# Performance work log

Measured on AMD Instinct MI355X. Metric: run time of the kernel, lower is better.

## Reference

```python
import jax, jax.numpy as jnp
import numpy as np

B, D, H, R = 64, 256, 512, 32
CLIP_VAL = 50.0


def setup_inputs() -> dict:
    key = jax.random.key(0)
    ks = jax.random.split(key, 12)
    inp = {
        "x": jax.random.normal(ks[0], (B, D), jnp.float32),
        "h": jax.random.normal(ks[1], (B, H), jnp.float32) * 0.1,
        "v": jax.random.normal(ks[2], (B, H), jnp.float32) * 0.1,
        "dU": jax.random.normal(ks[3], (B, H, H), jnp.float32) * 0.01,
        "trace_e": jax.random.normal(ks[4], (B, H), jnp.float32) * 0.1,
        "trace_E": jax.random.normal(ks[5], (B, H, H), jnp.float32) * 0.01,
        # parameters (per reset_parameter: xavier inits, zero biases)
        "x2h_w": jax.random.normal(ks[6], (H + R, D), jnp.float32) * (2.0 / (D + H + R)) ** 0.5,
        "x2h_b": jnp.zeros((H + R,), jnp.float32),
        "h2h_w": jax.random.normal(ks[7], (H + R, H), jnp.float32) * 1.5 * (2.0 / (H + H + R)) ** 0.5,
        "h2h_b": jnp.zeros((H + R,), jnp.float32),
        "alpha": jnp.ones((1, H, H), jnp.float32),
        "tau_v": -2.0 * jnp.ones((1, H), jnp.float32),
        "tau_e": -2.5 * jnp.ones((1, H), jnp.float32),
        "tau_U": -3.5 * jnp.ones((1,), jnp.float32),
        "tau_E": -3.5 * jnp.ones((1,), jnp.float32),
    }
    return inp


def _sgru_step(x, h, v, dU, trace_e, trace_E,
               x2h_w, x2h_b, h2h_w, h2h_b, alpha, tau_v, tau_e, tau_U, tau_E):
    Wx = x @ x2h_w.T + x2h_b            # [B, H+R]
    Wh = h @ h2h_w.T + h2h_b            # [B, H+R]
    alpha_r = jax.nn.relu(alpha)        # [1, H, H]
    # plastic fast-weight contribution: (relu(alpha)*dU) @ h
    plastic = jnp.einsum('bij,bj->bi', alpha_r * dU, h)  # [B, H]
    dv = Wx[:, :H] + Wh[:, :H] + plastic
    sv = jax.nn.sigmoid(tau_v)          # [1, H]
    v_new = (1.0 - sv) * v + sv * dv
    new_h = jax.nn.relu(v_new)          # activation='relu'
    # neuromodulatory scalar per batch element (sum over mod_rank channels)
    mod = jax.nn.relu(Wx[:, H:] + Wh[:, H:]).sum(axis=-1)  # [B]
    se = jax.nn.sigmoid(tau_e)
    new_trace_e = (1.0 - se) * trace_e + se * h             # [B, H]
    sE = jax.nn.sigmoid(tau_E)
    # antisymmetric eligibility trace update via outer products
    outer = new_h[:, :, None] * trace_e[:, None, :] - new_trace_e[:, :, None] * h[:, None, :]
    new_trace_E = (1.0 - sE) * trace_E + sE * outer         # [B, H, H]
    sU = jax.nn.sigmoid(tau_U)
    dU_new = (1.0 - sU) * dU + sU * mod[:, None, None] * new_trace_E
    # clip fast weights so total recurrent weight stays within [-clip, clip]
    W_hh = h2h_w[:H, :]                                     # [H, H]
    denom = alpha_r + 1e-8
    upper = jax.nn.relu(CLIP_VAL - W_hh) / denom            # [1, H, H]
    lower = -jax.nn.relu(CLIP_VAL + W_hh) / denom
    dU_new = jnp.maximum(jnp.minimum(dU_new, upper), lower)
    return v_new, new_h, dU_new, new_trace_e, new_trace_E


def reference(x, h, v, dU, trace_e, trace_E,
              x2h_w, x2h_b, h2h_w, h2h_b, alpha, tau_v, tau_e, tau_U, tau_E):
    return _sgru_step(x, h, v, dU, trace_e, trace_E,
                      x2h_w, x2h_b, h2h_w, h2h_b, alpha, tau_v, tau_e, tau_U, tau_E)
```

## Files before the change

### kernel.cpp

```cpp
#include <hip/hip_runtime.h>

#define BB 64
#define DD 256
#define HH 512
#define RR 32
#define CLIPV 50.0f

#define OUT_V   0
#define OUT_H   (BB * HH)
#define OUT_DU  (2 * BB * HH)
#define OUT_TE  (2 * BB * HH + BB * HH * HH)
#define OUT_TEE (3 * BB * HH + BB * HH * HH)

__device__ __forceinline__ float sigmoidf_(float x) {
    return 1.0f / (1.0f + expf(-x));
}

__global__ __launch_bounds__(256) void k_small(
    const float* __restrict__ x, const float* __restrict__ h, const float* __restrict__ v,
    const float* __restrict__ dU, const float* __restrict__ trace_e,
    const float* __restrict__ x2h_w, const float* __restrict__ x2h_b,
    const float* __restrict__ h2h_w, const float* __restrict__ h2h_b,
    const float* __restrict__ alpha,
    const float* __restrict__ tau_v, const float* __restrict__ tau_e,
    float* __restrict__ out, float* __restrict__ mod_ws)
{
    const int wave = blockIdx.x * 4 + (threadIdx.x >> 6);
    const int lane = threadIdx.x & 63;
    const int b = wave / (HH + RR);
    const int i = wave - b * (HH + RR);

    float4 xv = *reinterpret_cast<const float4*>(x + b * DD + lane * 4);
    float4 wv = *reinterpret_cast<const float4*>(x2h_w + i * DD + lane * 4);
    float s  = xv.x * wv.x + xv.y * wv.y + xv.z * wv.z + xv.w * wv.w;
    float pl = 0.0f;

    if (i < HH) {
        const float* dUrow = dU + (b * HH + i) * HH;
        const float* arow  = alpha + i * HH;
        #pragma unroll
        for (int p = 0; p < 2; ++p) {
            const int j0 = p * 256 + lane * 4;
            float4 hv  = *reinterpret_cast<const float4*>(h + b * HH + j0);
            float4 whv = *reinterpret_cast<const float4*>(h2h_w + i * HH + j0);
            s += hv.x * whv.x + hv.y * whv.y + hv.z * whv.z + hv.w * whv.w;
            float4 duv = *reinterpret_cast<const float4*>(dUrow + j0);
            float4 av  = *reinterpret_cast<const float4*>(arow + j0);
            pl += fmaxf(av.x, 0.f) * duv.x * hv.x
                + fmaxf(av.y, 0.f) * duv.y * hv.y
                + fmaxf(av.z, 0.f) * duv.z * hv.z
                + fmaxf(av.w, 0.f) * duv.w * hv.w;
        }
    } else {
        #pragma unroll
        for (int p = 0; p < 2; ++p) {
            const int j0 = p * 256 + lane * 4;
            float4 hv  = *reinterpret_cast<const float4*>(h + b * HH + j0);
            float4 whv = *reinterpret_cast<const float4*>(h2h_w + i * HH + j0);
            s += hv.x * whv.x + hv.y * whv.y + hv.z * whv.z + hv.w * whv.w;
        }
    }

    #pragma unroll
    for (int off = 32; off > 0; off >>= 1) {
        s  += __shfl_xor(s, off, 64);
        pl += __shfl_xor(pl, off, 64);
    }

    if (lane == 0) {
        s += x2h_b[i] + h2h_b[i];
        if (i < HH) {
            const int bi = b * HH + i;
            const float dv = s + pl;
            const float sv = sigmoidf_(tau_v[i]);
            const float vn = (1.f - sv) * v[bi] + sv * dv;
            out[OUT_V + bi] = vn;
            out[OUT_H + bi] = fmaxf(vn, 0.f);
            const float se = sigmoidf_(tau_e[i]);
            out[OUT_TE + bi] = (1.f - se) * trace_e[bi] + se * h[bi];
        } else {
            atomicAdd(mod_ws + b, fmaxf(s, 0.f));
        }
    }
}

__global__ __launch_bounds__(256) void k_big(
    const float* __restrict__ dU, const float* __restrict__ trace_E,
    const float* __restrict__ h, const float* __restrict__ trace_e,
    const float* __restrict__ alpha, const float* __restrict__ h2h_w,
    const float* __restrict__ tau_U, const float* __restrict__ tau_E,
    const float* __restrict__ mod_ws, float* __restrict__ out)
{
    const float sU = sigmoidf_(tau_U[0]);
    const float sE = sigmoidf_(tau_E[0]);
    const float omU = 1.f - sU, omE = 1.f - sE;
    const float* __restrict__ new_h  = out + OUT_H;
    const float* __restrict__ new_te = out + OUT_TE;
    float* __restrict__ out_dU = out + OUT_DU;
    float* __restrict__ out_tE = out + OUT_TEE;

    const int total = (BB * HH * HH) / 4;
    for (int idx = blockIdx.x * blockDim.x + threadIdx.x; idx < total;
         idx += gridDim.x * blockDim.x) {
        const int flat = idx << 2;
        const int b   = flat >> 18;
        const int rem = flat & ((1 << 18) - 1);
        const int i   = rem >> 9;
        const int j   = rem & (HH - 1);

        float4 tE = *reinterpret_cast<const float4*>(trace_E + flat);
        float4 du = *reinterpret_cast<const float4*>(dU + flat);
        float4 al = *reinterpret_cast<const float4*>(alpha + rem);
        float4 W  = *reinterpret_cast<const float4*>(h2h_w + rem);
        float4 hv = *reinterpret_cast<const float4*>(h + b * HH + j);
        float4 te = *reinterpret_cast<const float4*>(trace_e + b * HH + j);
        const float nh   = new_h[b * HH + i];
        const float nte  = new_te[b * HH + i];
        const float smod = sU * mod_ws[b];

        float4 rE, rU;
        #define COMP(c)                                                  \
        {                                                                \
            const float outer = nh * te.c - nte * hv.c;                  \
            const float nE    = omE * tE.c + sE * outer;                 \
            float dnew        = omU * du.c + smod * nE;                  \
            const float ar    = fmaxf(al.c, 0.f);                        \
            const float inv   = 1.0f / (ar + 1e-8f);                     \
            const float up    = fmaxf(CLIPV - W.c, 0.f) * inv;           \
            const float lo    = -fmaxf(CLIPV + W.c, 0.f) * inv;          \
            rE.c = nE;                                                   \
            rU.c = fmaxf(fminf(dnew, up), lo);                           \
        }
        COMP(x) COMP(y) COMP(z) COMP(w)
        #undef COMP

        *reinterpret_cast<float4*>(out_tE + flat) = rE;
        *reinterpret_cast<float4*>(out_dU + flat) = rU;
    }
}

extern "C" void kernel_launch(void* const* d_in, const int* in_sizes, int n_in,
                              void* d_out, int out_size, void* d_ws, size_t ws_size,
                              hipStream_t stream) {
    const float* x       = (const float*)d_in[0];
    const float* h       = (const float*)d_in[1];
    const float* v       = (const float*)d_in[2];
    const float* dU      = (const float*)d_in[3];
    const float* trace_e = (const float*)d_in[4];
    const float* trace_E = (const float*)d_in[5];
    const float* x2h_w   = (const float*)d_in[6];
    const float* x2h_b   = (const float*)d_in[7];
    const float* h2h_w   = (const float*)d_in[8];
    const float* h2h_b   = (const float*)d_in[9];
    const float* alpha   = (const float*)d_in[10];
    const float* tau_v   = (const float*)d_in[11];
    const float* tau_e   = (const float*)d_in[12];
    const float* tau_U   = (const float*)d_in[13];
    const float* tau_E   = (const float*)d_in[14];
    float* out    = (float*)d_out;
    float* mod_ws = (float*)d_ws;

    hipMemsetAsync(d_ws, 0, BB * sizeof(float), stream);

    const int waves = BB * (HH + RR);
    k_small<<<waves / 4, 256, 0, stream>>>(x, h, v, dU, trace_e, x2h_w, x2h_b,
                                           h2h_w, h2h_b, alpha, tau_v, tau_e,
                                           out, mod_ws);
    k_big<<<2048, 256, 0, stream>>>(dU, trace_E, h, trace_e, alpha, h2h_w,
                                    tau_U, tau_E, mod_ws, out);
}
```

Measured before the change: 288.0 us.

## Fuse plastic matvec with eligibility/fast-weight update to read dU once

New measurement: 281.6 us. 1.02x faster.

```diff
diff --git a/kernel.cpp b/kernel.cpp
--- a/kernel.cpp
+++ b/kernel.cpp
@@ -16,49 +16,77 @@
     return 1.0f / (1.0f + expf(-x));
 }
 
-__global__ __launch_bounds__(256) void k_small(
+__global__ __launch_bounds__(256) void k_mod(
+    const float* __restrict__ x, const float* __restrict__ h,
+    const float* __restrict__ x2h_w, const float* __restrict__ x2h_b,
+    const float* __restrict__ h2h_w, const float* __restrict__ h2h_b,
+    float* __restrict__ mod_ws)
+{
+    const int wave = blockIdx.x * 4 + (threadIdx.x >> 6);
+    const int lane = threadIdx.x & 63;
+    const int b = wave >> 5;
+    const int r = wave & (RR - 1);
+    const int i = HH + r;
+
+    float4 xv = *reinterpret_cast<const float4*>(x + b * DD + lane * 4);
+    float4 wv = *reinterpret_cast<const float4*>(x2h_w + i * DD + lane * 4);
+    float s = xv.x * wv.x + xv.y * wv.y + xv.z * wv.z + xv.w * wv.w;
+
+    #pragma unroll
+    for (int p = 0; p < 2; ++p) {
+        const int j0 = p * 256 + lane * 4;
+        float4 hv  = *reinterpret_cast<const float4*>(h + b * HH + j0);
+        float4 whv = *reinterpret_cast<const float4*>(h2h_w + i * HH + j0);
+        s += hv.x * whv.x + hv.y * whv.y + hv.z * whv.z + hv.w * whv.w;
+    }
+
+    #pragma unroll
+    for (int off = 32; off > 0; off >>= 1)
+        s += __shfl_xor(s, off, 64);
+
+    if (lane == 0) {
+        s += x2h_b[i] + h2h_b[i];
+        atomicAdd(mod_ws + b, fmaxf(s, 0.f));
+    }
+}
+
+__global__ __launch_bounds__(256) void k_fused(
     const float* __restrict__ x, const float* __restrict__ h, const float* __restrict__ v,
     const float* __restrict__ dU, const float* __restrict__ trace_e,
+    const float* __restrict__ trace_E,
     const float* __restrict__ x2h_w, const float* __restrict__ x2h_b,
     const float* __restrict__ h2h_w, const float* __restrict__ h2h_b,
     const float* __restrict__ alpha,
     const float* __restrict__ tau_v, const float* __restrict__ tau_e,
-    float* __restrict__ out, float* __restrict__ mod_ws)
+    const float* __restrict__ tau_U, const float* __restrict__ tau_E,
+    const float* __restrict__ mod_ws, float* __restrict__ out)
 {
     const int wave = blockIdx.x * 4 + (threadIdx.x >> 6);
     const int lane = threadIdx.x & 63;
-    const int b = wave / (HH + RR);
-    const int i = wave - b * (HH + RR);
+    const int b = wave >> 9;
+    const int i = wave & (HH - 1);
+    const int bi = b * HH + i;
 
     float4 xv = *reinterpret_cast<const float4*>(x + b * DD + lane * 4);
     float4 wv = *reinterpret_cast<const float4*>(x2h_w + i * DD + lane * 4);
     float s  = xv.x * wv.x + xv.y * wv.y + xv.z * wv.z + xv.w * wv.w;
     float pl = 0.0f;
 
-    if (i < HH) {
-        const float* dUrow = dU + (b * HH + i) * HH;
-        const float* arow  = alpha + i * HH;
-        #pragma unroll
-        for (int p = 0; p < 2; ++p) {
-            const int j0 = p * 256 + lane * 4;
-            float4 hv  = *reinterpret_cast<const float4*>(h + b * HH + j0);
-            float4 whv = *reinterpret_cast<const float4*>(h2h_w + i * HH + j0);
-            s += hv.x * whv.x + hv.y * whv.y + hv.z * whv.z + hv.w * whv.w;
-            float4 duv = *reinterpret_cast<const float4*>(dUrow + j0);
-            float4 av  = *reinterpret_cast<const float4*>(arow + j0);
-            pl += fmaxf(av.x, 0.f) * duv.x * hv.x
-                + fmaxf(av.y, 0.f) * duv.y * hv.y
-                + fmaxf(av.z, 0.f) * duv.z * hv.z
-                + fmaxf(av.w, 0.f) * duv.w * hv.w;
-        }
-    } else {
-        #pragma unroll
-        for (int p = 0; p < 2; ++p) {
-            const int j0 = p * 256 + lane * 4;
-            float4 hv  = *reinterpret_cast<const float4*>(h + b * HH + j0);
-            float4 whv = *reinterpret_cast<const float4*>(h2h_w + i * HH + j0);
-            s += hv.x * whv.x + hv.y * whv.y + hv.z * whv.z + hv.w * whv.w;
-        }
+    float4 hv[2], wh[2], du[2], av[2], te[2];
+    #pragma unroll
+    for (int p = 0; p < 2; ++p) {
+        const int j0 = p * 256 + lane * 4;
+        hv[p] = *reinterpret_cast<const float4*>(h + b * HH + j0);
+        wh[p] = *reinterpret_cast<const float4*>(h2h_w + i * HH + j0);
+        du[p] = *reinterpret_cast<const float4*>(dU + (size_t)bi * HH + j0);
+        av[p] = *reinterpret_cast<const float4*>(alpha + i * HH + j0);
+        te[p] = *reinterpret_cast<const float4*>(trace_e + b * HH + j0);
+        s += hv[p].x * wh[p].x + hv[p].y * wh[p].y
+           + hv[p].z * wh[p].z + hv[p].w * wh[p].w;
+        pl += fmaxf(av[p].x, 0.f) * du[p].x * hv[p].x
+            + fmaxf(av[p].y, 0.f) * du[p].y * hv[p].y
+            + fmaxf(av[p].z, 0.f) * du[p].z * hv[p].z
+            + fmaxf(av[p].w, 0.f) * du[p].w * hv[p].w;
     }
 
     #pragma unroll
@@ -67,75 +95,58 @@
         pl += __shfl_xor(pl, off, 64);
     }
 
+    s += x2h_b[i] + h2h_b[i];
+    const float dv = s + pl;
+    const float sv = sigmoidf_(tau_v[i]);
+    const float vn = (1.f - sv) * v[bi] + sv * dv;
+    const float nh = fmaxf(vn, 0.f);
+    const float se = sigmoidf_(tau_e[i]);
+    const float nte = (1.f - se) * trace_e[bi] + se * h[bi];
+
     if (lane == 0) {
-        s += x2h_b[i] + h2h_b[i];
-        if (i < HH) {
-            const int bi = b * HH + i;
-            const float dv = s + pl;
-            const float sv = sigmoidf_(tau_v[i]);
-            const float vn = (1.f - sv) * v[bi] + sv * dv;
-            out[OUT_V + bi] = vn;
-            out[OUT_H + bi] = fmaxf(vn, 0.f);
-            const float se = sigmoidf_(tau_e[i]);
-            out[OUT_TE + bi] = (1.f - se) * trace_e[bi] + se * h[bi];
-        } else {
-            atomicAdd(mod_ws + b, fmaxf(s, 0.f));
-        }
+        out[OUT_V  + bi] = vn;
+        out[OUT_H  + bi] = nh;
+        out[OUT_TE + bi] = nte;
     }
-}
 
-__global__ __launch_bounds__(256) void k_big(
-    const float* __restrict__ dU, const float* __restrict__ trace_E,
-    const float* __restrict__ h, const float* __restrict__ trace_e,
-    const float* __restrict__ alpha, const float* __restrict__ h2h_w,
-    const float* __restrict__ tau_U, const float* __restrict__ tau_E,
-    const float* __restrict__ mod_ws, float* __restrict__ out)
-{
-    const float sU = sigmoidf_(tau_U[0]);
-    const float sE = sigmoidf_(tau_E[0]);
+    const float sU  = sigmoidf_(tau_U[0]);
+    const float sE  = sigmoidf_(tau_E[0]);
     const float omU = 1.f - sU, omE = 1.f - sE;
-    const float* __restrict__ new_h  = out + OUT_H;
-    const float* __restrict__ new_te = out + OUT_TE;
+    const float smod = sU * mod_ws[b];
+
     float* __restrict__ out_dU = out + OUT_DU;
     float* __restrict__ out_tE = out + OUT_TEE;
 
-    const int total = (BB * HH * HH) / 4;
-    for (int idx = blockIdx.x * blockDim.x + threadIdx.x; idx < total;
-         idx += gridDim.x * blockDim.x) {
-        const int flat = idx << 2;
-        const int b   = flat >> 18;
-        const int rem = flat & ((1 << 18) - 1);
-        const int i   = rem >> 9;
-        const int j   = rem & (HH - 1);
-
+    #pragma unroll
+    for (int p = 0; p < 2; ++p) {
+        const int j0 = p * 256 + lane * 4;
+        const size_t flat = (size_t)bi * HH + j0;
         float4 tE = *reinterpret_cast<const float4*>(trace_E + flat);
-        float4 du = *reinterpret_cast<const float4*>(dU + flat);
-        float4 al = *reinterpret_cast<const float4*>(alpha + rem);
-        float4 W  = *reinterpret_cast<const float4*>(h2h_w + rem);
-        float4 hv = *reinterpret_cast<const float4*>(h + b * HH + j);
-        float4 te = *reinterpret_cast<const float4*>(trace_e + b * HH + j);
-        const float nh   = new_h[b * HH + i];
-        const float nte  = new_te[b * HH + i];
-        const float smod = sU * mod_ws[b];
 
         float4 rE, rU;
         #define COMP(c)                                                  \
         {                                                                \
-            const float outer = nh * te.c - nte * hv.c;                  \
+            const float outer = nh * te[p].c - nte * hv[p].c;            \
             const float nE    = omE * tE.c + sE * outer;                 \
-            float dnew        = omU * du.c + smod * nE;                  \
-            const float ar    = fmaxf(al.c, 0.f);                        \
+            const float dnew  = omU * du[p].c + smod * nE;               \
+            const float ar    = fmaxf(av[p].c, 0.f);                     \
             const float inv   = 1.0f / (ar + 1e-8f);                     \
-            const float up    = fmaxf(CLIPV - W.c, 0.f) * inv;           \
-            const float lo    = -fmaxf(CLIPV + W.c, 0.f) * inv;          \
+            const float up    = fmaxf(CLIPV - wh[p].c, 0.f) * inv;       \
+            const float lo    = -fmaxf(CLIPV + wh[p].c, 0.f) * inv;      \
             rE.c = nE;                                                   \
             rU.c = fmaxf(fminf(dnew, up), lo);                           \
         }
         COMP(x) COMP(y) COMP(z) COMP(w)
         #undef COMP
 
-        *reinterpret_cast<float4*>(out_tE + flat) = rE;
-        *reinterpret_cast<float4*>(out_dU + flat) = rU;
+        __builtin_nontemporal_store(rE.x, out_tE + flat + 0);
+        __builtin_nontemporal_store(rE.y, out_tE + flat + 1);
+        __builtin_nontemporal_store(rE.z, out_tE + flat + 2);
+        __builtin_nontemporal_store(rE.w, out_tE + flat + 3);
+        __builtin_nontemporal_store(rU.x, out_dU + flat + 0);
+        __builtin_nontemporal_store(rU.y, out_dU + flat + 1);
+        __builtin_nontemporal_store(rU.z, out_dU + flat + 2);
+        __builtin_nontemporal_store(rU.w, out_dU + flat + 3);
     }
 }
 
@@ -162,10 +173,9 @@
 
     hipMemsetAsync(d_ws, 0, BB * sizeof(float), stream);
 
-    const int waves = BB * (HH + RR);
-    k_small<<<waves / 4, 256, 0, stream>>>(x, h, v, dU, trace_e, x2h_w, x2h_b,
-                                           h2h_w, h2h_b, alpha, tau_v, tau_e,
-                                           out, mod_ws);
-    k_big<<<2048, 256, 0, stream>>>(dU, trace_E, h, trace_e, alpha, h2h_w,
-                                    tau_U, tau_E, mod_ws, out);
+    k_mod<<<512, 256, 0, stream>>>(x, h, x2h_w, x2h_b, h2h_w, h2h_b, mod_ws);
+
+    k_fused<<<8192, 256, 0, stream>>>(x, h, v, dU, trace_e, trace_E,
+                                      x2h_w, x2h_b, h2h_w, h2h_b, alpha,
+                                      tau_v, tau_e, tau_U, tau_E, mod_ws, out);
 }
```
